# Performance work log

Measured on AMD Instinct MI355X. Metric: run time of the kernel, lower is better.

## Reference

```python
import jax, jax.numpy as jnp
import numpy as np

B, S, M = 8, 2048, 256
D = 512          # input/memory feature dim
P = 512          # proj_dim
H = 8            # num_heads


def setup_inputs() -> dict:
    key = jax.random.key(0)
    ks = jax.random.split(key, 10)
    sc = 0.02
    return {
        "input_seq": jax.random.normal(ks[0], (B, S, D), jnp.float32),
        "memory_cells": jax.random.normal(ks[1], (B, M, D), jnp.float32),
        "Wk": jax.random.normal(ks[2], (D, P), jnp.float32) * sc,
        "bk": jnp.zeros((P,), jnp.float32),
        "Wv": jax.random.normal(ks[3], (D, P), jnp.float32) * sc,
        "bv": jnp.zeros((P,), jnp.float32),
        "Wq": jax.random.normal(ks[4], (H, D, P), jnp.float32) * sc,  # stacked per-head query Dense
        "bq": jnp.zeros((H, P), jnp.float32),
        "Wo": jax.random.normal(ks[5], (H * P, P), jnp.float32) * sc,
        "bo": jnp.zeros((P,), jnp.float32),
    }


def reference(input_seq, memory_cells, Wk, bk, Wv, bv, Wq, bq, Wo, bo):
    # shared key/value projections (multi-query: one K/V for all heads)
    ik = input_seq @ Wk + bk          # [B,S,P]
    mk = memory_cells @ Wk + bk       # [B,M,P]
    iv = input_seq @ Wv + bv          # [B,S,P]
    mv = memory_cells @ Wv + bv       # [B,M,P]

    # per-head queries from memory cells, all heads at once
    q = jnp.einsum('bmd,hdp->bhmp', memory_cells, Wq) + bq[None, :, None, :]  # [B,H,M,P]

    input_score = jnp.einsum('bhmp,bsp->bhms', q, ik)          # [B,H,M,S]
    self_score = jnp.sum(q * mk[:, None], axis=-1, keepdims=True)  # [B,H,M,1]
    score = jnp.concatenate([self_score, input_score], axis=-1)    # [B,H,M,S+1]
    score = score / jnp.sqrt(jnp.float32(P))
    attn = jax.nn.softmax(score, axis=-1)

    self_attn = attn[..., 0:1]                                  # [B,H,M,1]
    input_attn = attn[..., 1:]                                  # [B,H,M,S]
    val = jnp.einsum('bhms,bsp->bhmp', input_attn, iv) + self_attn * mv[:, None]

    # concat heads: [B,M,H*P]
    concat = jnp.transpose(val, (0, 2, 1, 3)).reshape(B, M, H * P)
    return concat @ Wo + bo           # [B,M,P]
```

## Files before the change

kernel.cpp:

```cpp
#include <hip/hip_runtime.h>

#define B_ 8
#define S_ 2048
#define M_ 256
#define D_ 512
#define P_ 512
#define H_ 8

#define SCALE 0.044194173824159216f

typedef __attribute__((ext_vector_type(8))) short bf16x8;
typedef __attribute__((ext_vector_type(4))) float f32x4;

static __device__ __forceinline__ float bf2f(short u) {
  union { float f; unsigned int i; } x;
  x.i = ((unsigned int)(unsigned short)u) << 16;
  return x.f;
}
static __device__ __forceinline__ short f2bf(float f) {
  union { float f; unsigned int i; } x;
  x.f = f;
  unsigned int r = (x.i + 0x7FFFu + ((x.i >> 16) & 1u)) >> 16;
  return (short)r;
}

static __device__ __forceinline__ void gll16(const short* g, short* l) {
  __builtin_amdgcn_global_load_lds(
      (const __attribute__((address_space(1))) void*)g,
      (__attribute__((address_space(3))) void*)l, 16, 0, 0);
}

#define LGKM_WAIT() asm volatile("s_waitcnt lgkmcnt(0)" ::: "memory")
#define VMLG_WAIT() asm volatile("s_waitcnt vmcnt(0) lgkmcnt(0)" ::: "memory")
#define RAW_BAR() do { asm volatile("" ::: "memory"); __builtin_amdgcn_s_barrier(); asm volatile("" ::: "memory"); } while (0)

__global__ __launch_bounds__(256) void cast_both(
    const float* __restrict__ inA, short* __restrict__ outA, int n4A,
    const float* __restrict__ inM, short* __restrict__ outM)
{
  int idx = blockIdx.x * 256 + threadIdx.x;
  const float* in = inA;
  short* out = outA;
  if (idx >= n4A) { idx -= n4A; in = inM; out = outM; }
  float4 v = ((const float4*)in)[idx];
  short o0 = f2bf(v.x), o1 = f2bf(v.y), o2 = f2bf(v.z), o3 = f2bf(v.w);
  uint2 pk;
  pk.x = (unsigned int)(unsigned short)o0 | ((unsigned int)(unsigned short)o1 << 16);
  pk.y = (unsigned int)(unsigned short)o2 | ((unsigned int)(unsigned short)o3 << 16);
  ((uint2*)out)[idx] = pk;
}

__global__ __launch_bounds__(256) void wtrans_all(
    const float* __restrict__ Wk, const float* __restrict__ Wv,
    const float* __restrict__ Wq,
    short* __restrict__ WkT, short* __restrict__ WvT, short* __restrict__ WqT)
{
  __shared__ float tile[32][33];
  const int t = threadIdx.x, tx = t & 31, ty = t >> 5;
  const int z = blockIdx.z;
  const float* inp;
  short* outp;
  if (z == 0)      { inp = Wk; outp = WkT; }
  else if (z == 1) { inp = Wv; outp = WvT; }
  else             { inp = Wq + (size_t)(z - 2) * 512 * 512;
                     outp = WqT + (size_t)(z - 2) * 512 * 512; }
  const int n0 = blockIdx.x * 32, k0 = blockIdx.y * 32;
#pragma unroll
  for (int i = 0; i < 4; ++i)
    tile[ty + 8 * i][tx] = inp[(size_t)(k0 + ty + 8 * i) * 512 + n0 + tx];
  __syncthreads();
#pragma unroll
  for (int i = 0; i < 4; ++i)
    outp[(size_t)(n0 + ty + 8 * i) * 512 + k0 + tx] = f2bf(tile[tx][ty + 8 * i]);
}

__global__ __launch_bounds__(256) void wtrans_wo(
    const float* __restrict__ in, short* __restrict__ out)
{
  __shared__ float tile[32][33];
  const int t = threadIdx.x, tx = t & 31, ty = t >> 5;
  const int n0 = blockIdx.x * 32, k0 = blockIdx.y * 32;
#pragma unroll
  for (int i = 0; i < 4; ++i)
    tile[ty + 8 * i][tx] = in[(size_t)(k0 + ty + 8 * i) * 512 + n0 + tx];
  __syncthreads();
#pragma unroll
  for (int i = 0; i < 4; ++i)
    out[(size_t)(n0 + ty + 8 * i) * 4096 + k0 + tx] = f2bf(tile[tx][ty + 8 * i]);
}

template<int MODE, int K, int N, int LDA, int LDB>
__global__ __launch_bounds__(256, 3) void gemm128(
    const short* __restrict__ Abase, const short* __restrict__ Bbase,
    const float* __restrict__ bias, void* __restrict__ Cv,
    const size_t aZ, const size_t bZ, const size_t cZ,
    float* __restrict__ Ls,
    const float* __restrict__ eselfp, const short* __restrict__ mvbp)
{
  __shared__ short As[4096];
  __shared__ short Bs[4096];
  const int t = threadIdx.x;
  const int w = t >> 6, lane = t & 63, qd = lane >> 4, ln = lane & 15;
  const int wm = (w & 1) * 64, wn = (w >> 1) * 64;

  const int n0 = blockIdx.x * 128;
  const int m0 = blockIdx.y * 128;
  const int z = blockIdx.z;
  const int bsel = z;

  const short* A  = Abase + (size_t)z * aZ;
  const short* Bp = Bbase + (size_t)bsel * bZ;

  const int rr = t >> 2, g0 = t & 3;
  const int gs0 = g0 ^ ((rr >> 1) & 3);
  const int gs1 = g0 ^ (((rr + 64) >> 1) & 3);
  const short* ga0 = A + (size_t)(m0 + rr) * LDA + gs0 * 8;
  const short* ga1 = A + (size_t)(m0 + rr + 64) * LDA + gs1 * 8;
  const short* gb0 = Bp + (size_t)(n0 + rr) * LDB + gs0 * 8;
  const short* gb1 = Bp + (size_t)(n0 + rr + 64) * LDB + gs1 * 8;

  int aoff[4], boff[4];
#pragma unroll
  for (int mt = 0; mt < 4; ++mt) {
    int r = wm + mt * 16 + ln;
    aoff[mt] = r * 32 + (qd ^ ((r >> 1) & 3)) * 8;
  }
#pragma unroll
  for (int nt = 0; nt < 4; ++nt) {
    int r = wn + nt * 16 + ln;
    boff[nt] = r * 32 + (qd ^ ((r >> 1) & 3)) * 8;
  }

  f32x4 acc[4][4];
#pragma unroll
  for (int mt = 0; mt < 4; ++mt)
#pragma unroll
    for (int nt = 0; nt < 4; ++nt) acc[mt][nt] = (f32x4){0.f, 0.f, 0.f, 0.f};

  for (int kc = 0; kc < K; kc += 32) {
    __syncthreads();
    gll16(ga0 + kc, &As[w * 512]);
    gll16(ga1 + kc, &As[2048 + w * 512]);
    gll16(gb0 + kc, &Bs[w * 512]);
    gll16(gb1 + kc, &Bs[2048 + w * 512]);
    __syncthreads();

    bf16x8 af[4], bfr[4];
#pragma unroll
    for (int mt = 0; mt < 4; ++mt) af[mt] = *(const bf16x8*)&As[aoff[mt]];
#pragma unroll
    for (int nt = 0; nt < 4; ++nt) bfr[nt] = *(const bf16x8*)&Bs[boff[nt]];
#pragma unroll
    for (int mt = 0; mt < 4; ++mt)
#pragma unroll
      for (int nt = 0; nt < 4; ++nt)
        acc[mt][nt] = __builtin_amdgcn_mfma_f32_16x16x32_bf16(af[mt], bfr[nt], acc[mt][nt], 0, 0, 0);
  }

  if constexpr (MODE == 5) {
#pragma unroll
    for (int nt = 0; nt < 4; ++nt) {
      const int col = n0 + wn + nt * 16 + ln;
#pragma unroll
      for (int mt = 0; mt < 4; ++mt)
#pragma unroll
        for (int r = 0; r < 4; ++r) {
          const int row = m0 + wm + mt * 16 + qd * 4 + r;
          ((float*)Cv)[(size_t)z * cZ + (size_t)row * N + col] = acc[mt][nt][r];
        }
    }
  } else {
#pragma unroll
    for (int nt = 0; nt < 4; ++nt) {
      const int col = n0 + wn + nt * 16 + ln;
      const float bc = bias[512 * z + col];
#pragma unroll
      for (int mt = 0; mt < 4; ++mt)
#pragma unroll
        for (int r = 0; r < 4; ++r) {
          const int row = m0 + wm + mt * 16 + qd * 4 + r;
          const int bidx = row >> 8, ml = row & 255;
          ((short*)Cv)[((size_t)(bidx * H_ + z) * M_ + ml) * N + col] = f2bf(acc[mt][nt][r] + bc);
        }
    }
  }
}

template<int NKT>
__global__ __launch_bounds__(512, 2) void qk256(
    const short* __restrict__ Abase, const short* __restrict__ Bbase,
    short* __restrict__ Eb, float* __restrict__ Ls)
{
  __shared__ short lds[65536];
  const int t = threadIdx.x;
  const int w = t >> 6, lane = t & 63, qd = lane >> 4, ln = lane & 15;
  const int wr = w >> 2, wc = w & 3;
  const int b = blockIdx.x;
  const int n0 = blockIdx.y * 256, m0 = blockIdx.z * 256;

  const short* A  = Abase + (size_t)b * (2048 * 512) + (size_t)m0 * 512;
  const short* Bp = Bbase + (size_t)b * (2048 * 512) + (size_t)n0 * 512;

  const int s0 = w * 64 + lane, s1 = s0 + 512;
  const int sr0 = s0 >> 3, sc0 = ((s0 & 7) ^ (sr0 & 7)) * 8;
  const int sr1 = s1 >> 3, sc1 = ((s1 & 7) ^ (sr1 & 7)) * 8;
  auto stage = [&](const short* g, short* lbase) {
    gll16(g + (size_t)sr0 * 512 + sc0, lbase + w * 512);
    gll16(g + (size_t)sr1 * 512 + sc1, lbase + 4096 + w * 512);
  };

  const int cq0 = ((qd    ) ^ (ln & 7)) * 8;
  const int cq1 = ((4 + qd) ^ (ln & 7)) * 8;
  const int brow = (wc & 1) * 64;

  f32x4 acc[8][4];
#pragma unroll
  for (int i = 0; i < 8; ++i)
#pragma unroll
    for (int j = 0; j < 4; ++j) acc[i][j] = (f32x4){0.f, 0.f, 0.f, 0.f};

  stage(A,              &lds[0]);
  stage(A + 128 * 512,  &lds[8192]);
  stage(Bp,             &lds[32768]);
  stage(Bp + 128 * 512, &lds[32768 + 8192]);
  asm volatile("s_waitcnt vmcnt(0)" ::: "memory");
  __builtin_amdgcn_s_barrier();

#pragma unroll 1
  for (int kt = 0; kt < NKT; ++kt) {
    const int p = kt & 1;
    short* Ah = &lds[p * 16384 + wr * 8192];
    short* Bh = &lds[32768 + p * 16384 + (wc >> 1) * 8192];

    bf16x8 a0[8], b0[4];
#pragma unroll
    for (int j = 0; j < 4; ++j)
      b0[j] = *(const bf16x8*)&Bh[(brow + j * 16 + ln) * 64 + cq0];
#pragma unroll
    for (int mt = 0; mt < 8; ++mt)
      a0[mt] = *(const bf16x8*)&Ah[(mt * 16 + ln) * 64 + cq0];
    if (kt + 1 < NKT) {
      stage(A  + (size_t)(kt + 1) * 64,             &lds[(p ^ 1) * 16384]);
      stage(A  + 128 * 512 + (size_t)(kt + 1) * 64, &lds[(p ^ 1) * 16384 + 8192]);
      stage(Bp + (size_t)(kt + 1) * 64,             &lds[32768 + (p ^ 1) * 16384]);
      stage(Bp + 128 * 512 + (size_t)(kt + 1) * 64, &lds[32768 + (p ^ 1) * 16384 + 8192]);
    }
    __builtin_amdgcn_s_setprio(1);
#pragma unroll
    for (int mt = 0; mt < 8; ++mt)
#pragma unroll
      for (int j = 0; j < 4; ++j)
        acc[mt][j] = __builtin_amdgcn_mfma_f32_16x16x32_bf16(a0[mt], b0[j], acc[mt][j], 0, 0, 0);
    __builtin_amdgcn_s_setprio(0);

    bf16x8 a1[8], b1[4];
#pragma unroll
    for (int j = 0; j < 4; ++j)
      b1[j] = *(const bf16x8*)&Bh[(brow + j * 16 + ln) * 64 + cq1];
#pragma unroll
    for (int mt = 0; mt < 8; ++mt)
      a1[mt] = *(const bf16x8*)&Ah[(mt * 16 + ln) * 64 + cq1];
    __builtin_amdgcn_s_setprio(1);
#pragma unroll
    for (int mt = 0; mt < 8; ++mt)
#pragma unroll
      for (int j = 0; j < 4; ++j)
        acc[mt][j] = __builtin_amdgcn_mfma_f32_16x16x32_bf16(a1[mt], b1[j], acc[mt][j], 0, 0, 0);
    __builtin_amdgcn_s_setprio(0);

    VMLG_WAIT();
    RAW_BAR();
  }

#pragma unroll
  for (int i = 0; i < 8; ++i)
#pragma unroll
    for (int j = 0; j < 4; ++j)
#pragma unroll
      for (int r = 0; r < 4; ++r)
        acc[i][j][r] = __expf(acc[i][j][r] * SCALE);
#pragma unroll
  for (int i = 0; i < 8; ++i)
#pragma unroll
    for (int r = 0; r < 4; ++r) {
      float rs = acc[i][0][r] + acc[i][1][r] + acc[i][2][r] + acc[i][3][r];
      rs += __shfl_xor(rs, 1);
      rs += __shfl_xor(rs, 2);
      rs += __shfl_xor(rs, 4);
      rs += __shfl_xor(rs, 8);
      if (ln == 0) {
        const int row = m0 + wr * 128 + i * 16 + qd * 4 + r;
        atomicAdd(&Ls[(size_t)b * 2048 + row], rs);
      }
    }
#pragma unroll
  for (int i = 0; i < 8; ++i)
#pragma unroll
    for (int j = 0; j < 4; ++j)
#pragma unroll
      for (int r = 0; r < 4; ++r) {
        const int row = wr * 128 + i * 16 + qd * 4 + r;
        const int col = wc * 64 + j * 16 + ln;
        lds[row * 256 + (col ^ ((row & 7) << 3))] = f2bf(acc[i][j][r]);
      }
  LGKM_WAIT();
  RAW_BAR();
  short* Cb = Eb + (size_t)b * 2048 * 2048;
#pragma unroll
  for (int it = 0; it < 16; ++it) {
    const int flat = it * 512 + t;
    const int row = flat >> 5, c = flat & 31;
    bf16x8 v = *(const bf16x8*)&lds[row * 256 + ((c ^ (row & 7)) * 8)];
    *(bf16x8*)(Cb + (size_t)(m0 + row) * 2048 + n0 + c * 8) = v;
  }
}

template<int NKT>
__global__ __launch_bounds__(512, 2) void pv128(
    const short* __restrict__ Abase, const short* __restrict__ Bbase,
    short* __restrict__ valb, const float* __restrict__ Ls,
    const float* __restrict__ eselfp, const short* __restrict__ mvbp)
{
  __shared__ short lds[49152];
  const int t = threadIdx.x;
  const int w = t >> 6, lane = t & 63, qd = lane >> 4, ln = lane & 15;
  const int wr = w >> 1, wc = w & 1;
  const int b = blockIdx.x;
  const int n0 = blockIdx.y * 128;
  const int bz = blockIdx.z;
  const int m0 = bz * 256;

  const short* A  = Abase + (size_t)b * (2048 * 2048) + (size_t)m0 * 2048;
  const short* Bp = Bbase + (size_t)b * (512 * 2048) + (size_t)n0 * 2048;

  const int s0 = w * 64 + lane, s1 = s0 + 512;
  const int sr0 = s0 >> 3, sc0 = ((s0 & 7) ^ (sr0 & 7)) * 8;
  const int sr1 = s1 >> 3, sc1 = ((s1 & 7) ^ (sr1 & 7)) * 8;
  auto stage = [&](const short* g, short* lbase) {
    gll16(g + (size_t)sr0 * 2048 + sc0, lbase + w * 512);
    gll16(g + (size_t)sr1 * 2048 + sc1, lbase + 4096 + w * 512);
  };

  const int cq0 = ((qd    ) ^ (ln & 7)) * 8;
  const int cq1 = ((4 + qd) ^ (ln & 7)) * 8;

  f32x4 acc[4][4];
#pragma unroll
  for (int i = 0; i < 4; ++i)
#pragma unroll
    for (int j = 0; j < 4; ++j) acc[i][j] = (f32x4){0.f, 0.f, 0.f, 0.f};

  stage(A,               &lds[0]);
  stage(A + 128 * 2048,  &lds[8192]);
  stage(Bp,              &lds[32768]);
  asm volatile("s_waitcnt vmcnt(0)" ::: "memory");
  __builtin_amdgcn_s_barrier();

#pragma unroll 1
  for (int kt = 0; kt < NKT; ++kt) {
    const int p = kt & 1;
    short* Ah = &lds[p * 16384 + (wr >> 1) * 8192 + (wr & 1) * 4096];
    short* Bh = &lds[32768 + p * 8192];

    bf16x8 a0[4], b0[4];
#pragma unroll
    for (int j = 0; j < 4; ++j)
      b0[j] = *(const bf16x8*)&Bh[(wc * 64 + j * 16 + ln) * 64 + cq0];
#pragma unroll
    for (int mt = 0; mt < 4; ++mt)
      a0[mt] = *(const bf16x8*)&Ah[(mt * 16 + ln) * 64 + cq0];
    if (kt + 1 < NKT) {
      stage(A  + (size_t)(kt + 1) * 64,              &lds[(p ^ 1) * 16384]);
      stage(A  + 128 * 2048 + (size_t)(kt + 1) * 64, &lds[(p ^ 1) * 16384 + 8192]);
      stage(Bp + (size_t)(kt + 1) * 64,              &lds[32768 + (p ^ 1) * 8192]);
    }
    __builtin_amdgcn_s_setprio(1);
#pragma unroll
    for (int mt = 0; mt < 4; ++mt)
#pragma unroll
      for (int j = 0; j < 4; ++j)
        acc[mt][j] = __builtin_amdgcn_mfma_f32_16x16x32_bf16(a0[mt], b0[j], acc[mt][j], 0, 0, 0);
    __builtin_amdgcn_s_setprio(0);

    bf16x8 a1[4], b1[4];
#pragma unroll
    for (int j = 0; j < 4; ++j)
      b1[j] = *(const bf16x8*)&Bh[(wc * 64 + j * 16 + ln) * 64 + cq1];
#pragma unroll
    for (int mt = 0; mt < 4; ++mt)
      a1[mt] = *(const bf16x8*)&Ah[(mt * 16 + ln) * 64 + cq1];
    __builtin_amdgcn_s_setprio(1);
#pragma unroll
    for (int mt = 0; mt < 4; ++mt)
#pragma unroll
      for (int j = 0; j < 4; ++j)
        acc[mt][j] = __builtin_amdgcn_mfma_f32_16x16x32_bf16(a1[mt], b1[j], acc[mt][j], 0, 0, 0);
    __builtin_amdgcn_s_setprio(0);

    VMLG_WAIT();
    RAW_BAR();
  }

#pragma unroll
  for (int mt = 0; mt < 4; ++mt)
#pragma unroll
    for (int r = 0; r < 4; ++r) {
      const int row = wr * 64 + mt * 16 + qd * 4 + r;
      const float es  = eselfp[(size_t)b * 2048 + m0 + row];
      const float inv = 1.f / (es + Ls[(size_t)b * 2048 + m0 + row]);
      const short* mvr = mvbp + ((size_t)(b * 256 + row)) * 512;
#pragma unroll
      for (int j = 0; j < 4; ++j) {
        const int lcol = wc * 64 + j * 16 + ln;
        const float v = (acc[mt][j][r] + es * bf2f(mvr[n0 + lcol])) * inv;
        lds[row * 128 + (lcol ^ ((row & 7) << 3))] = f2bf(v);
      }
    }
  LGKM_WAIT();
  RAW_BAR();
#pragma unroll
  for (int it = 0; it < 8; ++it) {
    const int flat = it * 512 + t;
    const int row = flat >> 4, c = flat & 15;
    bf16x8 v = *(const bf16x8*)&lds[row * 128 + ((c ^ (row & 7)) * 8)];
    *(bf16x8*)(valb + ((size_t)(b * 256 + row)) * 4096 + (size_t)bz * 512 + n0 + c * 8) = v;
  }
}

template<bool TRANSV>
__global__ __launch_bounds__(256, 3) void proj_kv(
    const short* __restrict__ A,
    const short* __restrict__ WkT, const short* __restrict__ WvT,
    const float* __restrict__ bk, const float* __restrict__ bv,
    short* __restrict__ Ck, short* __restrict__ Cvv)
{
  __shared__ short Sh[8192];
  short* As  = Sh;
  short* Bks = Sh + 4096;
  short* Bvs = Sh + 6144;
  const int t = threadIdx.x;
  const int w = t >> 6, lane = t & 63, qd = lane >> 4, ln = lane & 15;
  const int n0 = blockIdx.x * 64, m0 = blockIdx.y * 128;
  const int wm = (w & 1) * 64, wn2 = (w >> 1) * 32;

  const int rr = t >> 2, g0 = t & 3;
  const int gs0 = g0 ^ ((rr >> 1) & 3);
  const int gs1 = g0 ^ (((rr + 64) >> 1) & 3);
  const short* ga0 = A + (size_t)(m0 + rr) * 512 + gs0 * 8;
  const short* ga1 = A + (size_t)(m0 + rr + 64) * 512 + gs1 * 8;
  const short* gbk = WkT + (size_t)(n0 + rr) * 512 + gs0 * 8;
  const short* gbv = WvT + (size_t)(n0 + rr) * 512 + gs0 * 8;

  int aoff[4], boff[2];
#pragma unroll
  for (int mt = 0; mt < 4; ++mt) {
    int r = wm + mt * 16 + ln;
    aoff[mt] = r * 32 + (qd ^ ((r >> 1) & 3)) * 8;
  }
#pragma unroll
  for (int nt = 0; nt < 2; ++nt) {
    int r = wn2 + nt * 16 + ln;
    boff[nt] = r * 32 + (qd ^ ((r >> 1) & 3)) * 8;
  }

  f32x4 accK[4][2], accV[4][2];
#pragma unroll
  for (int mt = 0; mt < 4; ++mt)
#pragma unroll
    for (int nt = 0; nt < 2; ++nt) {
      accK[mt][nt] = (f32x4){0.f, 0.f, 0.f, 0.f};
      accV[mt][nt] = (f32x4){0.f, 0.f, 0.f, 0.f};
    }

  for (int kc = 0; kc < 512; kc += 32) {
    __syncthreads();
    gll16(ga0 + kc, &As[w * 512]);
    gll16(ga1 + kc, &As[2048 + w * 512]);
    gll16(gbk + kc, &Bks[w * 512]);
    gll16(gbv + kc, &Bvs[w * 512]);
    __syncthreads();

    bf16x8 af[4], bkf[2], bvf[2];
#pragma unroll
    for (int mt = 0; mt < 4; ++mt) af[mt] = *(const bf16x8*)&As[aoff[mt]];
#pragma unroll
    for (int nt = 0; nt < 2; ++nt) {
      bkf[nt] = *(const bf16x8*)&Bks[boff[nt]];
      bvf[nt] = *(const bf16x8*)&Bvs[boff[nt]];
    }
#pragma unroll
    for (int mt = 0; mt < 4; ++mt)
#pragma unroll
      for (int nt = 0; nt < 2; ++nt) {
        accK[mt][nt] = __builtin_amdgcn_mfma_f32_16x16x32_bf16(af[mt], bkf[nt], accK[mt][nt], 0, 0, 0);
        accV[mt][nt] = __builtin_amdgcn_mfma_f32_16x16x32_bf16(af[mt], bvf[nt], accV[mt][nt], 0, 0, 0);
      }
  }

#pragma unroll
  for (int nt = 0; nt < 2; ++nt) {
    const int col = n0 + wn2 + nt * 16 + ln;
    const float bc = bk[col];
#pragma unroll
    for (int mt = 0; mt < 4; ++mt)
#pragma unroll
      for (int r = 0; r < 4; ++r) {
        const int row = m0 + wm + mt * 16 + qd * 4 + r;
        Ck[(size_t)row * 512 + col] = f2bf(accK[mt][nt][r] + bc);
      }
  }

  if constexpr (!TRANSV) {
#pragma unroll
    for (int nt = 0; nt < 2; ++nt) {
      const int col = n0 + wn2 + nt * 16 + ln;
      const float bc = bv[col];
#pragma unroll
      for (int mt = 0; mt < 4; ++mt)
#pragma unroll
        for (int r = 0; r < 4; ++r) {
          const int row = m0 + wm + mt * 16 + qd * 4 + r;
          Cvv[(size_t)row * 512 + col] = f2bf(accV[mt][nt][r] + bc);
        }
    }
  } else {
    __syncthreads();
    short* ep = &Sh[w * 1280];
    const int lr = lane >> 1, lc16 = (lane & 1) * 16;
#pragma unroll
    for (int pass = 0; pass < 2; ++pass) {
#pragma unroll
      for (int mh = 0; mh < 2; ++mh) {
        const int mt = pass * 2 + mh;
#pragma unroll
        for (int nt = 0; nt < 2; ++nt) {
          const float bc = bv[n0 + wn2 + nt * 16 + ln];
#pragma unroll
          for (int r = 0; r < 4; ++r)
            ep[(nt * 16 + ln) * 40 + mh * 16 + qd * 4 + r] = f2bf(accV[mt][nt][r] + bc);
        }
      }
      LGKM_WAIT();
      const int srow0 = m0 + wm + pass * 32;
      const int bidx = srow0 >> 11;
      const int sloc = (srow0 & 2047) + lc16;
      const int pcol = n0 + wn2 + lr;
      short* outp = Cvv + (size_t)bidx * P_ * S_ + (size_t)pcol * S_ + sloc;
      *(bf16x8*)outp = *(const bf16x8*)&ep[lr * 40 + lc16];
      *(bf16x8*)(outp + 8) = *(const bf16x8*)&ep[lr * 40 + lc16 + 8];
      LGKM_WAIT();
    }
  }
}

__global__ __launch_bounds__(256) void reduce_wo(
    const float* __restrict__ partial, const float* __restrict__ bo,
    float* __restrict__ out)
{
  const int idx4 = blockIdx.x * 256 + threadIdx.x;
  float4 s = ((const float4*)bo)[idx4 & 127];
#pragma unroll
  for (int zz = 0; zz < 4; ++zz) {
    float4 p = ((const float4*)partial)[(size_t)zz * 262144 + idx4];
    s.x += p.x; s.y += p.y; s.z += p.z; s.w += p.w;
  }
  ((float4*)out)[idx4] = s;
}

__global__ __launch_bounds__(256) void selfscore(
    const short* __restrict__ qb, const short* __restrict__ mkb,
    float* __restrict__ eself, float* __restrict__ Ls)
{
  const int z = blockIdx.x, t = threadIdx.x;
  const short* qr = qb + ((size_t)z * M_ + t) * P_;
  const short* mr = mkb + ((size_t)(z >> 3) * M_ + t) * P_;
  float s = 0.f;
#pragma unroll 8
  for (int c = 0; c < P_; c += 8) {
    bf16x8 qv = *(const bf16x8*)(qr + c);
    bf16x8 mv = *(const bf16x8*)(mr + c);
#pragma unroll
    for (int j = 0; j < 8; ++j) s += bf2f(qv[j]) * bf2f(mv[j]);
  }
  eself[(size_t)z * M_ + t] = __expf(s * SCALE);
  Ls[(size_t)z * M_ + t] = 0.f;
}

extern "C" void kernel_launch(void* const* d_in, const int* in_sizes, int n_in,
                              void* d_out, int out_size, void* d_ws, size_t ws_size,
                              hipStream_t stream) {
  const float* input_seq = (const float*)d_in[0];
  const float* memcells  = (const float*)d_in[1];
  const float* Wk = (const float*)d_in[2];
  const float* bk = (const float*)d_in[3];
  const float* Wv = (const float*)d_in[4];
  const float* bv = (const float*)d_in[5];
  const float* Wq = (const float*)d_in[6];
  const float* bq = (const float*)d_in[7];
  const float* Wo = (const float*)d_in[8];
  const float* bo = (const float*)d_in[9];
  float* out = (float*)d_out;

  short* ws = (short*)d_ws;
  size_t o = 0;
  short* valb = ws + o; o += (size_t)B_ * M_ * H_ * P_;
  short* WoT  = ws + o; o += (size_t)(H_ * P_) * P_;
  short* mvb  = ws + o; o += (size_t)B_ * M_ * P_;
  short* mkb  = ws + o; o += (size_t)B_ * M_ * P_;
  short* qb   = ws + o; o += (size_t)B_ * H_ * M_ * P_;
  short* ivT  = ws + o; o += (size_t)B_ * P_ * S_;
  short* ikb  = ws + o; o += (size_t)B_ * S_ * P_;
  float* partial = (float*)(ws + o); o += (size_t)B_ * H_ * M_ * P_;
  float* eself = (float*)(ws + o); o += 2 * (size_t)B_ * H_ * M_;
  float* Ls    = (float*)(ws + o); o += 2 * (size_t)B_ * H_ * M_;
  short* region2 = ws + o;
  short* Ab  = region2;
  short* Mb  = Ab + (size_t)B_ * S_ * D_;
  short* WkT = Mb + (size_t)B_ * M_ * D_;
  short* WvT = WkT + (size_t)D_ * P_;
  short* WqT = WvT + (size_t)D_ * P_;
  short* Eb  = region2;

  dim3 blk(256);

  const int n4A = B_ * S_ * D_ / 4;
  const int n4M = B_ * M_ * D_ / 4;
  cast_both<<<dim3((n4A + n4M) / 256), blk, 0, stream>>>(input_seq, Ab, n4A, memcells, Mb);
  wtrans_all<<<dim3(16, 16, 10), blk, 0, stream>>>(Wk, Wv, Wq, WkT, WvT, WqT);
  wtrans_wo<<<dim3(16, 128), blk, 0, stream>>>(Wo, WoT);

  proj_kv<true><<<dim3(8, 128), blk, 0, stream>>>(Ab, WkT, WvT, bk, bv, ikb, ivT);
  proj_kv<false><<<dim3(8, 16), blk, 0, stream>>>(Mb, WkT, WvT, bk, bv, mkb, mvb);

  gemm128<1, 512, 512, 512, 512><<<dim3(4, 16, 8), blk, 0, stream>>>(
      Mb, WqT, bq, qb, 0, (size_t)D_ * P_, 0, nullptr, nullptr, nullptr);

  selfscore<<<dim3(64), blk, 0, stream>>>(qb, mkb, eself, Ls);

  qk256<8><<<dim3(8, 8, 8), dim3(512), 0, stream>>>(qb, ikb, Eb, Ls);

  pv128<32><<<dim3(8, 4, 8), dim3(512), 0, stream>>>(Eb, ivT, valb, Ls, eself, mvb);

  gemm128<5, 1024, 512, 4096, 4096><<<dim3(4, 16, 4), blk, 0, stream>>>(
      valb, WoT, nullptr, partial, 1024, 1024,
      (size_t)2048 * 512, nullptr, nullptr, nullptr);
  reduce_wo<<<dim3(1024), blk, 0, stream>>>(partial, bo, out);
}
```

Measured before the change: 305.8 us.

## Triple-buffer LDS tiles in qk256 and pv128 with two-deep async prefetch

Both attention GEMM kernels move from double-buffered to triple-buffered LDS staging with rotating read, next and write buffers. Global-to-LDS loads are issued two k-steps ahead, and partial vmcnt waits keep one stage in flight across each barrier. qk256 also halves its k-tile to 32 (so it runs twice as many iterations) with a new XOR swizzle and precomputed fragment offsets. The aim is to hide global-load latency behind MFMA work, at the cost of more LDS in pv128 and more barriers per k in qk256.

```diff
diff --git a/kernel.cpp b/kernel.cpp
--- a/kernel.cpp
+++ b/kernel.cpp
@@ -31,7 +31,6 @@
 }
 
 #define LGKM_WAIT() asm volatile("s_waitcnt lgkmcnt(0)" ::: "memory")
-#define VMLG_WAIT() asm volatile("s_waitcnt vmcnt(0) lgkmcnt(0)" ::: "memory")
 #define RAW_BAR() do { asm volatile("" ::: "memory"); __builtin_amdgcn_s_barrier(); asm volatile("" ::: "memory"); } while (0)
 
 __global__ __launch_bounds__(256) void cast_both(
@@ -201,17 +200,29 @@
   const short* A  = Abase + (size_t)b * (2048 * 512) + (size_t)m0 * 512;
   const short* Bp = Bbase + (size_t)b * (2048 * 512) + (size_t)n0 * 512;
 
-  const int s0 = w * 64 + lane, s1 = s0 + 512;
-  const int sr0 = s0 >> 3, sc0 = ((s0 & 7) ^ (sr0 & 7)) * 8;
-  const int sr1 = s1 >> 3, sc1 = ((s1 & 7) ^ (sr1 & 7)) * 8;
-  auto stage = [&](const short* g, short* lbase) {
-    gll16(g + (size_t)sr0 * 512 + sc0, lbase + w * 512);
-    gll16(g + (size_t)sr1 * 512 + sc1, lbase + 4096 + w * 512);
+  const int srow = t >> 2;
+  const int scol = ((t & 3) ^ ((srow >> 1) & 3)) * 8;
+  const short* gsA = A  + (size_t)srow * 512 + scol;
+  const short* gsB = Bp + (size_t)srow * 512 + scol;
+
+  auto stageA = [&](const short* g, short* l) {
+    gll16(g,             l + w * 512);
+    gll16(g + 128 * 512, l + 4096 + w * 512);
   };
-
-  const int cq0 = ((qd    ) ^ (ln & 7)) * 8;
-  const int cq1 = ((4 + qd) ^ (ln & 7)) * 8;
-  const int brow = (wc & 1) * 64;
+  auto stageB = [&](const short* g, short* l) {
+    gll16(g,             l + w * 512);
+    gll16(g + 128 * 512, l + 4096 + w * 512);
+  };
+
+  const int fq = (qd ^ ((ln >> 1) & 3)) * 8;
+  int aoff[8], boff[4];
+#pragma unroll
+  for (int mt = 0; mt < 8; ++mt) aoff[mt] = (mt * 16 + ln) * 32 + fq;
+#pragma unroll
+  for (int j = 0; j < 4; ++j)    boff[j]  = (j * 16 + ln) * 32 + fq;
+
+  short* Ar = &lds[0];     short* An = &lds[8192];  short* Aw = &lds[16384];
+  short* Br = &lds[24576]; short* Bn = &lds[32768]; short* Bw = &lds[40960];
 
   f32x4 acc[8][4];
 #pragma unroll
@@ -219,57 +230,41 @@
 #pragma unroll
     for (int j = 0; j < 4; ++j) acc[i][j] = (f32x4){0.f, 0.f, 0.f, 0.f};
 
-  stage(A,              &lds[0]);
-  stage(A + 128 * 512,  &lds[8192]);
-  stage(Bp,             &lds[32768]);
-  stage(Bp + 128 * 512, &lds[32768 + 8192]);
-  asm volatile("s_waitcnt vmcnt(0)" ::: "memory");
+  stageA(gsA,      Ar); stageB(gsB,      Br);
+  stageA(gsA + 32, An); stageB(gsB + 32, Bn);
+  asm volatile("s_waitcnt vmcnt(4)" ::: "memory");
   __builtin_amdgcn_s_barrier();
 
 #pragma unroll 1
   for (int kt = 0; kt < NKT; ++kt) {
-    const int p = kt & 1;
-    short* Ah = &lds[p * 16384 + wr * 8192];
-    short* Bh = &lds[32768 + p * 16384 + (wc >> 1) * 8192];
-
-    bf16x8 a0[8], b0[4];
-#pragma unroll
-    for (int j = 0; j < 4; ++j)
-      b0[j] = *(const bf16x8*)&Bh[(brow + j * 16 + ln) * 64 + cq0];
+    short* Ah = Ar + wr * 4096;
+    short* Bh = Br + wc * 2048;
+
+    bf16x8 a[8], bfr[4];
+#pragma unroll
+    for (int j = 0; j < 4; ++j) bfr[j] = *(const bf16x8*)&Bh[boff[j]];
+#pragma unroll
+    for (int mt = 0; mt < 8; ++mt) a[mt] = *(const bf16x8*)&Ah[aoff[mt]];
+
+    if (kt + 2 < NKT) {
+      stageA(gsA + (size_t)(kt + 2) * 32, Aw);
+      stageB(gsB + (size_t)(kt + 2) * 32, Bw);
+    }
+
+    __builtin_amdgcn_s_setprio(1);
 #pragma unroll
     for (int mt = 0; mt < 8; ++mt)
-      a0[mt] = *(const bf16x8*)&Ah[(mt * 16 + ln) * 64 + cq0];
-    if (kt + 1 < NKT) {
-      stage(A  + (size_t)(kt + 1) * 64,             &lds[(p ^ 1) * 16384]);
-      stage(A  + 128 * 512 + (size_t)(kt + 1) * 64, &lds[(p ^ 1) * 16384 + 8192]);
-      stage(Bp + (size_t)(kt + 1) * 64,             &lds[32768 + (p ^ 1) * 16384]);
-      stage(Bp + 128 * 512 + (size_t)(kt + 1) * 64, &lds[32768 + (p ^ 1) * 16384 + 8192]);
-    }
-    __builtin_amdgcn_s_setprio(1);
-#pragma unroll
-    for (int mt = 0; mt < 8; ++mt)
 #pragma unroll
       for (int j = 0; j < 4; ++j)
-        acc[mt][j] = __builtin_amdgcn_mfma_f32_16x16x32_bf16(a0[mt], b0[j], acc[mt][j], 0, 0, 0);
+        acc[mt][j] = __builtin_amdgcn_mfma_f32_16x16x32_bf16(a[mt], bfr[j], acc[mt][j], 0, 0, 0);
     __builtin_amdgcn_s_setprio(0);
 
-    bf16x8 a1[8], b1[4];
-#pragma unroll
-    for (int j = 0; j < 4; ++j)
-      b1[j] = *(const bf16x8*)&Bh[(brow + j * 16 + ln) * 64 + cq1];
-#pragma unroll
-    for (int mt = 0; mt < 8; ++mt)
-      a1[mt] = *(const bf16x8*)&Ah[(mt * 16 + ln) * 64 + cq1];
-    __builtin_amdgcn_s_setprio(1);
-#pragma unroll
-    for (int mt = 0; mt < 8; ++mt)
-#pragma unroll
-      for (int j = 0; j < 4; ++j)
-        acc[mt][j] = __builtin_amdgcn_mfma_f32_16x16x32_bf16(a1[mt], b1[j], acc[mt][j], 0, 0, 0);
-    __builtin_amdgcn_s_setprio(0);
-
-    VMLG_WAIT();
+    if (kt + 2 < NKT) { asm volatile("s_waitcnt vmcnt(4) lgkmcnt(0)" ::: "memory"); }
+    else              { asm volatile("s_waitcnt vmcnt(0) lgkmcnt(0)" ::: "memory"); }
     RAW_BAR();
+
+    short* tA = Ar; Ar = An; An = Aw; Aw = tA;
+    short* tB = Br; Br = Bn; Bn = Bw; Bw = tB;
   }
 
 #pragma unroll
@@ -321,7 +316,7 @@
     short* __restrict__ valb, const float* __restrict__ Ls,
     const float* __restrict__ eselfp, const short* __restrict__ mvbp)
 {
-  __shared__ short lds[49152];
+  __shared__ short lds[73728];
   const int t = threadIdx.x;
   const int w = t >> 6, lane = t & 63, qd = lane >> 4, ln = lane & 15;
   const int wr = w >> 1, wc = w & 1;
@@ -344,23 +339,28 @@
   const int cq0 = ((qd    ) ^ (ln & 7)) * 8;
   const int cq1 = ((4 + qd) ^ (ln & 7)) * 8;
 
+  short* Ar = &lds[0];     short* An = &lds[16384]; short* Aw = &lds[32768];
+  short* Br = &lds[49152]; short* Bn = &lds[57344]; short* Bw = &lds[65536];
+
   f32x4 acc[4][4];
 #pragma unroll
   for (int i = 0; i < 4; ++i)
 #pragma unroll
     for (int j = 0; j < 4; ++j) acc[i][j] = (f32x4){0.f, 0.f, 0.f, 0.f};
 
-  stage(A,               &lds[0]);
-  stage(A + 128 * 2048,  &lds[8192]);
-  stage(Bp,              &lds[32768]);
-  asm volatile("s_waitcnt vmcnt(0)" ::: "memory");
+  stage(A,                   Ar);
+  stage(A + 128 * 2048,      Ar + 8192);
+  stage(Bp,                  Br);
+  stage(A + 64,              An);
+  stage(A + 128 * 2048 + 64, An + 8192);
+  stage(Bp + 64,             Bn);
+  asm volatile("s_waitcnt vmcnt(6)" ::: "memory");
   __builtin_amdgcn_s_barrier();
 
 #pragma unroll 1
   for (int kt = 0; kt < NKT; ++kt) {
-    const int p = kt & 1;
-    short* Ah = &lds[p * 16384 + (wr >> 1) * 8192 + (wr & 1) * 4096];
-    short* Bh = &lds[32768 + p * 8192];
+    short* Ah = Ar + (wr >> 1) * 8192 + (wr & 1) * 4096;
+    short* Bh = Br;
 
     bf16x8 a0[4], b0[4];
 #pragma unroll
@@ -369,11 +369,13 @@
 #pragma unroll
     for (int mt = 0; mt < 4; ++mt)
       a0[mt] = *(const bf16x8*)&Ah[(mt * 16 + ln) * 64 + cq0];
-    if (kt + 1 < NKT) {
-      stage(A  + (size_t)(kt + 1) * 64,              &lds[(p ^ 1) * 16384]);
-      stage(A  + 128 * 2048 + (size_t)(kt + 1) * 64, &lds[(p ^ 1) * 16384 + 8192]);
-      stage(Bp + (size_t)(kt + 1) * 64,              &lds[32768 + (p ^ 1) * 8192]);
-    }
+
+    if (kt + 2 < NKT) {
+      stage(A  + (size_t)(kt + 2) * 64,              Aw);
+      stage(A  + 128 * 2048 + (size_t)(kt + 2) * 64, Aw + 8192);
+      stage(Bp + (size_t)(kt + 2) * 64,              Bw);
+    }
+
     __builtin_amdgcn_s_setprio(1);
 #pragma unroll
     for (int mt = 0; mt < 4; ++mt)
@@ -397,8 +399,12 @@
         acc[mt][j] = __builtin_amdgcn_mfma_f32_16x16x32_bf16(a1[mt], b1[j], acc[mt][j], 0, 0, 0);
     __builtin_amdgcn_s_setprio(0);
 
-    VMLG_WAIT();
+    if (kt + 2 < NKT) { asm volatile("s_waitcnt vmcnt(6) lgkmcnt(0)" ::: "memory"); }
+    else              { asm volatile("s_waitcnt vmcnt(0) lgkmcnt(0)" ::: "memory"); }
     RAW_BAR();
+
+    short* tA = Ar; Ar = An; An = Aw; Aw = tA;
+    short* tB = Br; Br = Bn; Bn = Bw; Bw = tB;
   }
 
 #pragma unroll
@@ -637,7 +643,7 @@
 
   selfscore<<<dim3(64), blk, 0, stream>>>(qb, mkb, eself, Ls);
 
-  qk256<8><<<dim3(8, 8, 8), dim3(512), 0, stream>>>(qb, ikb, Eb, Ls);
+  qk256<16><<<dim3(8, 8, 8), dim3(512), 0, stream>>>(qb, ikb, Eb, Ls);
 
   pv128<32><<<dim3(8, 4, 8), dim3(512), 0, stream>>>(Eb, ivT, valb, Ls, eself, mvb);
 
```

After: 300.5 us. No clear change (-1.7%).

## Double-buffer LDS in gemm128 and proj_kv, triple-buffer pv128

Applied to the files above, without the earlier changes.

The generic gemm128 and proj_kv kernels move from single-buffered LDS loads with two barriers per k-step to a double-buffered scheme: each step prefetches the next tile while the current one runs through MFMA, and sets priority around the MFMA block. pv128 goes from two to three LDS buffers, with two tiles in flight and vmcnt-based waits, to hide more global-load latency. LDS use per block grows (pv128 to about 144KB), which may cut occupancy, and gemm128's launch bound of 3 blocks may no longer fit.

```diff
diff --git a/kernel.cpp b/kernel.cpp
--- a/kernel.cpp
+++ b/kernel.cpp
@@ -97,8 +97,8 @@
     float* __restrict__ Ls,
     const float* __restrict__ eselfp, const short* __restrict__ mvbp)
 {
-  __shared__ short As[4096];
-  __shared__ short Bs[4096];
+  __shared__ short As[8192];
+  __shared__ short Bs[8192];
   const int t = threadIdx.x;
   const int w = t >> 6, lane = t & 63, qd = lane >> 4, ln = lane & 15;
   const int wm = (w & 1) * 64, wn = (w >> 1) * 64;
@@ -106,10 +106,9 @@
   const int n0 = blockIdx.x * 128;
   const int m0 = blockIdx.y * 128;
   const int z = blockIdx.z;
-  const int bsel = z;
 
   const short* A  = Abase + (size_t)z * aZ;
-  const short* Bp = Bbase + (size_t)bsel * bZ;
+  const short* Bp = Bbase + (size_t)z * bZ;
 
   const int rr = t >> 2, g0 = t & 3;
   const int gs0 = g0 ^ ((rr >> 1) & 3);
@@ -137,24 +136,43 @@
 #pragma unroll
     for (int nt = 0; nt < 4; ++nt) acc[mt][nt] = (f32x4){0.f, 0.f, 0.f, 0.f};
 
+  gll16(ga0, &As[w * 512]);
+  gll16(ga1, &As[2048 + w * 512]);
+  gll16(gb0, &Bs[w * 512]);
+  gll16(gb1, &Bs[2048 + w * 512]);
+  asm volatile("s_waitcnt vmcnt(0)" ::: "memory");
+  __builtin_amdgcn_s_barrier();
+
+#pragma unroll 1
   for (int kc = 0; kc < K; kc += 32) {
-    __syncthreads();
-    gll16(ga0 + kc, &As[w * 512]);
-    gll16(ga1 + kc, &As[2048 + w * 512]);
-    gll16(gb0 + kc, &Bs[w * 512]);
-    gll16(gb1 + kc, &Bs[2048 + w * 512]);
-    __syncthreads();
+    const int p = (kc >> 5) & 1;
+    short* Ap = &As[p * 4096];
+    short* Bq = &Bs[p * 4096];
 
     bf16x8 af[4], bfr[4];
 #pragma unroll
-    for (int mt = 0; mt < 4; ++mt) af[mt] = *(const bf16x8*)&As[aoff[mt]];
-#pragma unroll
-    for (int nt = 0; nt < 4; ++nt) bfr[nt] = *(const bf16x8*)&Bs[boff[nt]];
+    for (int mt = 0; mt < 4; ++mt) af[mt] = *(const bf16x8*)&Ap[aoff[mt]];
+#pragma unroll
+    for (int nt = 0; nt < 4; ++nt) bfr[nt] = *(const bf16x8*)&Bq[boff[nt]];
+
+    if (kc + 32 < K) {
+      const int nb = (p ^ 1) * 4096;
+      gll16(ga0 + kc + 32, &As[nb + w * 512]);
+      gll16(ga1 + kc + 32, &As[nb + 2048 + w * 512]);
+      gll16(gb0 + kc + 32, &Bs[nb + w * 512]);
+      gll16(gb1 + kc + 32, &Bs[nb + 2048 + w * 512]);
+    }
+
+    __builtin_amdgcn_s_setprio(1);
 #pragma unroll
     for (int mt = 0; mt < 4; ++mt)
 #pragma unroll
       for (int nt = 0; nt < 4; ++nt)
         acc[mt][nt] = __builtin_amdgcn_mfma_f32_16x16x32_bf16(af[mt], bfr[nt], acc[mt][nt], 0, 0, 0);
+    __builtin_amdgcn_s_setprio(0);
+
+    VMLG_WAIT();
+    RAW_BAR();
   }
 
   if constexpr (MODE == 5) {
@@ -321,7 +339,7 @@
     short* __restrict__ valb, const float* __restrict__ Ls,
     const float* __restrict__ eselfp, const short* __restrict__ mvbp)
 {
-  __shared__ short lds[49152];
+  __shared__ short lds[73728];
   const int t = threadIdx.x;
   const int w = t >> 6, lane = t & 63, qd = lane >> 4, ln = lane & 15;
   const int wr = w >> 1, wc = w & 1;
@@ -344,23 +362,28 @@
   const int cq0 = ((qd    ) ^ (ln & 7)) * 8;
   const int cq1 = ((4 + qd) ^ (ln & 7)) * 8;
 
+  short* Ar = &lds[0];     short* An = &lds[16384]; short* Aw = &lds[32768];
+  short* Br = &lds[49152]; short* Bn = &lds[57344]; short* Bw = &lds[65536];
+
   f32x4 acc[4][4];
 #pragma unroll
   for (int i = 0; i < 4; ++i)
 #pragma unroll
     for (int j = 0; j < 4; ++j) acc[i][j] = (f32x4){0.f, 0.f, 0.f, 0.f};
 
-  stage(A,               &lds[0]);
-  stage(A + 128 * 2048,  &lds[8192]);
-  stage(Bp,              &lds[32768]);
-  asm volatile("s_waitcnt vmcnt(0)" ::: "memory");
+  stage(A,                   Ar);
+  stage(A + 128 * 2048,      Ar + 8192);
+  stage(Bp,                  Br);
+  stage(A + 64,              An);
+  stage(A + 128 * 2048 + 64, An + 8192);
+  stage(Bp + 64,             Bn);
+  asm volatile("s_waitcnt vmcnt(6)" ::: "memory");
   __builtin_amdgcn_s_barrier();
 
 #pragma unroll 1
   for (int kt = 0; kt < NKT; ++kt) {
-    const int p = kt & 1;
-    short* Ah = &lds[p * 16384 + (wr >> 1) * 8192 + (wr & 1) * 4096];
-    short* Bh = &lds[32768 + p * 8192];
+    short* Ah = Ar + (wr >> 1) * 8192 + (wr & 1) * 4096;
+    short* Bh = Br;
 
     bf16x8 a0[4], b0[4];
 #pragma unroll
@@ -369,11 +392,13 @@
 #pragma unroll
     for (int mt = 0; mt < 4; ++mt)
       a0[mt] = *(const bf16x8*)&Ah[(mt * 16 + ln) * 64 + cq0];
-    if (kt + 1 < NKT) {
-      stage(A  + (size_t)(kt + 1) * 64,              &lds[(p ^ 1) * 16384]);
-      stage(A  + 128 * 2048 + (size_t)(kt + 1) * 64, &lds[(p ^ 1) * 16384 + 8192]);
-      stage(Bp + (size_t)(kt + 1) * 64,              &lds[32768 + (p ^ 1) * 8192]);
-    }
+
+    if (kt + 2 < NKT) {
+      stage(A  + (size_t)(kt + 2) * 64,              Aw);
+      stage(A  + 128 * 2048 + (size_t)(kt + 2) * 64, Aw + 8192);
+      stage(Bp + (size_t)(kt + 2) * 64,              Bw);
+    }
+
     __builtin_amdgcn_s_setprio(1);
 #pragma unroll
     for (int mt = 0; mt < 4; ++mt)
@@ -397,8 +422,12 @@
         acc[mt][j] = __builtin_amdgcn_mfma_f32_16x16x32_bf16(a1[mt], b1[j], acc[mt][j], 0, 0, 0);
     __builtin_amdgcn_s_setprio(0);
 
-    VMLG_WAIT();
+    if (kt + 2 < NKT) { asm volatile("s_waitcnt vmcnt(6) lgkmcnt(0)" ::: "memory"); }
+    else              { asm volatile("s_waitcnt vmcnt(0) lgkmcnt(0)" ::: "memory"); }
     RAW_BAR();
+
+    short* tA = Ar; Ar = An; An = Aw; Aw = tA;
+    short* tB = Br; Br = Bn; Bn = Bw; Bw = tB;
   }
 
 #pragma unroll
@@ -434,10 +463,7 @@
     const float* __restrict__ bk, const float* __restrict__ bv,
     short* __restrict__ Ck, short* __restrict__ Cvv)
 {
-  __shared__ short Sh[8192];
-  short* As  = Sh;
-  short* Bks = Sh + 4096;
-  short* Bvs = Sh + 6144;
+  __shared__ short Sh[16384];
   const int t = threadIdx.x;
   const int w = t >> 6, lane = t & 63, qd = lane >> 4, ln = lane & 15;
   const int n0 = blockIdx.x * 64, m0 = blockIdx.y * 128;
@@ -472,22 +498,35 @@
       accV[mt][nt] = (f32x4){0.f, 0.f, 0.f, 0.f};
     }
 
+  gll16(ga0, &Sh[w * 512]);
+  gll16(ga1, &Sh[2048 + w * 512]);
+  gll16(gbk, &Sh[4096 + w * 512]);
+  gll16(gbv, &Sh[6144 + w * 512]);
+  asm volatile("s_waitcnt vmcnt(0)" ::: "memory");
+  __builtin_amdgcn_s_barrier();
+
+#pragma unroll 1
   for (int kc = 0; kc < 512; kc += 32) {
-    __syncthreads();
-    gll16(ga0 + kc, &As[w * 512]);
-    gll16(ga1 + kc, &As[2048 + w * 512]);
-    gll16(gbk + kc, &Bks[w * 512]);
-    gll16(gbv + kc, &Bvs[w * 512]);
-    __syncthreads();
+    const int base = ((kc >> 5) & 1) * 8192;
 
     bf16x8 af[4], bkf[2], bvf[2];
 #pragma unroll
-    for (int mt = 0; mt < 4; ++mt) af[mt] = *(const bf16x8*)&As[aoff[mt]];
+    for (int mt = 0; mt < 4; ++mt) af[mt] = *(const bf16x8*)&Sh[base + aoff[mt]];
 #pragma unroll
     for (int nt = 0; nt < 2; ++nt) {
-      bkf[nt] = *(const bf16x8*)&Bks[boff[nt]];
-      bvf[nt] = *(const bf16x8*)&Bvs[boff[nt]];
-    }
+      bkf[nt] = *(const bf16x8*)&Sh[base + 4096 + boff[nt]];
+      bvf[nt] = *(const bf16x8*)&Sh[base + 6144 + boff[nt]];
+    }
+
+    if (kc + 32 < 512) {
+      const int nb = base ^ 8192;
+      gll16(ga0 + kc + 32, &Sh[nb + w * 512]);
+      gll16(ga1 + kc + 32, &Sh[nb + 2048 + w * 512]);
+      gll16(gbk + kc + 32, &Sh[nb + 4096 + w * 512]);
+      gll16(gbv + kc + 32, &Sh[nb + 6144 + w * 512]);
+    }
+
+    __builtin_amdgcn_s_setprio(1);
 #pragma unroll
     for (int mt = 0; mt < 4; ++mt)
 #pragma unroll
@@ -495,6 +534,10 @@
         accK[mt][nt] = __builtin_amdgcn_mfma_f32_16x16x32_bf16(af[mt], bkf[nt], accK[mt][nt], 0, 0, 0);
         accV[mt][nt] = __builtin_amdgcn_mfma_f32_16x16x32_bf16(af[mt], bvf[nt], accV[mt][nt], 0, 0, 0);
       }
+    __builtin_amdgcn_s_setprio(0);
+
+    VMLG_WAIT();
+    RAW_BAR();
   }
 
 #pragma unroll
```

Measured after the change: 303.0 us. About the same (-0.9%).
